# Optimization experiments

Measured on AMD Instinct MI355X. Metric: run time of the kernel, lower is better.

The kernel has to match this reference:

```python
import jax, jax.numpy as jnp
import numpy as np


def setup_inputs() -> dict:
    key = jax.random.key(0)
    k1, k2, k3, k4 = jax.random.split(key, 4)
    b, c_in, t, h, w = 8, 64, 16, 64, 64
    c_out, kh, kw = 64, 3, 3
    x = jax.random.normal(k1, (b, c_in, t, h, w), dtype=jnp.float32)
    alpha = jax.random.uniform(k2, (b, c_in, t, 1, 1), dtype=jnp.float32)
    fan_in = c_in * kh * kw
    weight = jax.random.normal(k3, (c_out, c_in, kh, kw), dtype=jnp.float32) / np.sqrt(fan_in)
    bias = jax.random.normal(k4, (c_out,), dtype=jnp.float32) * 0.05
    return {"x": x, "alpha": alpha, "weight": weight, "bias": bias}


def reference(x, alpha, weight, bias):
    # x: (b, c_in, t, h, w); alpha: (b, c_in, t, 1, 1)
    # weight: (c_out, c_in, kh, kw); bias: (c_out,)
    b, c_in, t, h, w = x.shape
    c_out, _, kh, kw = weight.shape
    pad = ((kh // 2, kh // 2), (kw // 2, kw // 2))  # padding=1 for 3x3
    # per-(b,t) calibrated weights: alpha scales the c_in dim (cal_dim='cin')
    a = jnp.transpose(alpha[..., 0, 0], (0, 2, 1))          # (b, t, c_in)
    w_bt = a[:, :, None, :, None, None] * weight[None, None]  # (b, t, c_out, c_in, kh, kw)
    xs = jnp.transpose(x, (0, 2, 1, 3, 4)).reshape(b * t, 1, c_in, h, w)
    ws = w_bt.reshape(b * t, c_out, c_in, kh, kw)

    def conv_one(xi, wi):
        return jax.lax.conv_general_dilated(
            xi, wi, window_strides=(1, 1), padding=pad,
            dimension_numbers=("NCHW", "OIHW", "NCHW"))[0]

    out = jax.vmap(conv_one)(xs, ws)                          # (b*t, c_out, h, w)
    out = out + bias[None, :, None, None]
    out = out.reshape(b, t, c_out, h, w).transpose(0, 2, 1, 3, 4)
    return out  # (b, c_out, t, h, w)
```

## Files before the change

### kernel.cpp

```cpp
#include <hip/hip_runtime.h>


#define CIN  64
#define COUT 64
#define TT   16
#define BB   8
#define HH   64
#define WW   64

typedef __attribute__((ext_vector_type(8))) short bf16x8;
typedef __attribute__((ext_vector_type(4))) float f32x4;

__device__ __forceinline__ unsigned short f2bf(float f) {
    union { float f; unsigned u; } v; v.f = f;
    unsigned r = (v.u + 0x7FFF + ((v.u >> 16) & 1)) >> 16;
    return (unsigned short)r;
}

__global__ __launch_bounds__(256) void prep_x(const float* __restrict__ x,
                                              const float* __restrict__ alpha,
                                              int4* __restrict__ xh) {
    __shared__ float ls[64 * 66];
    const int blk = blockIdx.x;
    const int h   = blk & 63;
    const int bt  = blk >> 6;
    const int t   = bt & 15;
    const int b   = bt >> 4;
    const int tid = threadIdx.x;

#pragma unroll
    for (int it = 0; it < 4; ++it) {
        int idx4 = tid + it * 256;
        int ci   = idx4 >> 4;
        int w4   = (idx4 & 15) * 4;
        float a  = alpha[(b * CIN + ci) * TT + t];
        const float* gp = x + (((b * CIN + ci) * TT + t) * HH + h) * WW + w4;
        float4 v = *(const float4*)gp;
        ls[(w4 + 0) * 66 + ci] = v.x * a;
        ls[(w4 + 1) * 66 + ci] = v.y * a;
        ls[(w4 + 2) * 66 + ci] = v.z * a;
        ls[(w4 + 3) * 66 + ci] = v.w * a;
    }
    __syncthreads();

#pragma unroll
    for (int it = 0; it < 2; ++it) {
        int tau  = tid + it * 256;
        int w    = tau >> 3;
        int slot = tau & 7;
        int g    = slot ^ (w & 7);
        const float* p = &ls[w * 66 + g * 8];
        float2 p0 = *(const float2*)(p + 0);
        float2 p1 = *(const float2*)(p + 2);
        float2 p2 = *(const float2*)(p + 4);
        float2 p3 = *(const float2*)(p + 6);
        int4 o;
        o.x = (int)f2bf(p0.x) | ((int)f2bf(p0.y) << 16);
        o.y = (int)f2bf(p1.x) | ((int)f2bf(p1.y) << 16);
        o.z = (int)f2bf(p2.x) | ((int)f2bf(p2.y) << 16);
        o.w = (int)f2bf(p3.x) | ((int)f2bf(p3.y) << 16);
        xh[((bt * 64 + h) * 64 + w) * 8 + slot] = o;
    }
}

__global__ __launch_bounds__(256) void prep_w(const float* __restrict__ wgt,
                                              unsigned short* __restrict__ wb) {
    int idx = blockIdx.x * 256 + threadIdx.x;
    if (idx < COUT * CIN * 9) {
        int co  = idx / (CIN * 9);
        int r   = idx - co * (CIN * 9);
        int ci  = r / 9;
        int tap = r - ci * 9;
        int slot = (ci >> 3) ^ (co & 7);
        wb[((tap * COUT + co) * 8 + slot) * 8 + (ci & 7)] = f2bf(wgt[idx]);
    }
}

__global__ __launch_bounds__(256) void conv2(const short* __restrict__ xh,
                                             const short* __restrict__ wb,
                                             const float* __restrict__ bias,
                                             float* __restrict__ out) {
    __shared__ __align__(16) short xs[4][66 * 64];
    __shared__ __align__(16) short wl[2][64 * 64];

    const int blk   = blockIdx.x;
    const int ytile = blk & 31;
    const int bt    = blk >> 5;
    const int t     = bt & 15;
    const int b     = bt >> 4;
    const int y0    = ytile * 2;
    const int tid   = threadIdx.x;
    const int wave  = tid >> 6;
    const int lane  = tid & 63;

    {
        const int r  = wave;
        const int gy = y0 - 1 + r;
        int4* dst = (int4*)xs[r];
        if ((unsigned)gy < HH) {
            const int4* src = (const int4*)(xh + (bt * 64 + gy) * 64 * 64);
            int4* d = (int4*)(xs[r] + 64);
#pragma unroll
            for (int it = 0; it < 8; ++it) d[it * 64 + lane] = src[it * 64 + lane];
            int4 z = {0, 0, 0, 0};
            if (lane < 8)       dst[lane] = z;
            else if (lane < 16) ((int4*)(xs[r] + 4160))[lane - 8] = z;
        } else {
            int4 z = {0, 0, 0, 0};
#pragma unroll
            for (int it = 0; it < 9; ++it) {
                int idx = it * 64 + lane;
                if (idx < 528) dst[idx] = z;
            }
        }
    }
    {
        const int4* src = (const int4*)wb;
        int4* d = (int4*)wl[0];
        d[tid] = src[tid];
        d[tid + 256] = src[tid + 256];
    }
    __syncthreads();

    f32x4 acc[4][2] = {};
    const int ywave = wave >> 1;
    const int wseg  = (wave & 1) * 32;
    const int co_l  = lane & 15;
    const int kg    = lane >> 4;

    for (int tap = 0; tap < 9; ++tap) {
        const int cur = tap & 1;
        int4 wp0, wp1;
        if (tap < 8) {
            const int4* src = (const int4*)(wb + (tap + 1) * 4096);
            wp0 = src[tid];
            wp1 = src[tid + 256];
        }
        const int ky = tap / 3;
        const int dx = (tap - 3 * ky) - 1;
        const short* xrow = xs[ywave + ky];
        const short* wcur = wl[cur];

#pragma unroll
        for (int kc = 0; kc < 2; ++kc) {
            const int g = kc * 4 + kg;
            bf16x8 af[4];
#pragma unroll
            for (int m = 0; m < 4; ++m) {
                int co   = m * 16 + co_l;
                int slot = g ^ (co & 7);
                af[m] = *(const bf16x8*)(wcur + co * 64 + slot * 8);
            }
            bf16x8 bfr[2];
#pragma unroll
            for (int nt = 0; nt < 2; ++nt) {
                int w    = wseg + nt * 16 + co_l;
                int wx   = w + dx;
                int slot = g ^ (wx & 7);
                bfr[nt] = *(const bf16x8*)(xrow + (wx + 1) * 64 + slot * 8);
            }
#pragma unroll
            for (int m = 0; m < 4; ++m)
#pragma unroll
                for (int nt = 0; nt < 2; ++nt)
                    acc[m][nt] = __builtin_amdgcn_mfma_f32_16x16x32_bf16(
                        af[m], bfr[nt], acc[m][nt], 0, 0, 0);
        }

        if (tap < 8) {
            int4* d = (int4*)wl[cur ^ 1];
            d[tid] = wp0;
            d[tid + 256] = wp1;
        }
        __syncthreads();
    }

    const int y = y0 + ywave;
#pragma unroll
    for (int m = 0; m < 4; ++m) {
#pragma unroll
        for (int r = 0; r < 4; ++r) {
            int co = m * 16 + (lane >> 4) * 4 + r;
            float bv = bias[co];
            float* op = out + (((b * COUT + co) * TT + t) * HH + y) * WW;
#pragma unroll
            for (int nt = 0; nt < 2; ++nt) {
                int w = wseg + nt * 16 + co_l;
                op[w] = acc[m][nt][r] + bv;
            }
        }
    }
}

extern "C" void kernel_launch(void* const* d_in, const int* in_sizes, int n_in,
                              void* d_out, int out_size, void* d_ws, size_t ws_size,
                              hipStream_t stream) {
    const float* x      = (const float*)d_in[0];
    const float* alpha  = (const float*)d_in[1];
    const float* weight = (const float*)d_in[2];
    const float* bias   = (const float*)d_in[3];
    float* out          = (float*)d_out;

    unsigned short* wb = (unsigned short*)d_ws;
    short* xhat = (short*)((char*)d_ws + (128 << 10));

    hipLaunchKernelGGL(prep_w, dim3(144), dim3(256), 0, stream, weight, wb);
    hipLaunchKernelGGL(prep_x, dim3(BB * TT * HH), dim3(256), 0, stream,
                       x, alpha, (int4*)xhat);
    hipLaunchKernelGGL(conv2, dim3(BB * TT * (HH / 2)), dim3(256), 0, stream,
                       xhat, (const short*)wb, bias, out);
}
```

Baseline: 284.5 us.

## Keep conv weights in registers and process four output rows per block

The conv kernel now loads each wave's full weight slice (all 9 taps, 32 output channels) into registers once, then loops over four output rows instead of two. This removes the shared-memory weight double-buffering and the per-tap barriers. Weights are stored unswizzled in global memory and read directly. prep_x changes its LDS row stride to 67 and uses scalar reads, to cut bank conflicts. The trade-off is heavy register pressure from 36 bf16x8 fragments under launch_bounds(256,2), a sequential per-row loop with fewer accumulators per wave, and half as many blocks.

```diff
diff --git a/kernel.cpp b/kernel.cpp
--- a/kernel.cpp
+++ b/kernel.cpp
@@ -11,16 +11,15 @@
 typedef __attribute__((ext_vector_type(8))) short bf16x8;
 typedef __attribute__((ext_vector_type(4))) float f32x4;
 
-__device__ __forceinline__ unsigned short f2bf(float f) {
+__device__ __forceinline__ unsigned int f2bf(float f) {
     union { float f; unsigned u; } v; v.f = f;
-    unsigned r = (v.u + 0x7FFF + ((v.u >> 16) & 1)) >> 16;
-    return (unsigned short)r;
+    return (v.u + 0x7FFF + ((v.u >> 16) & 1)) >> 16;
 }
 
 __global__ __launch_bounds__(256) void prep_x(const float* __restrict__ x,
                                               const float* __restrict__ alpha,
                                               int4* __restrict__ xh) {
-    __shared__ float ls[64 * 66];
+    __shared__ float ls[64 * 67];
     const int blk = blockIdx.x;
     const int h   = blk & 63;
     const int bt  = blk >> 6;
@@ -36,10 +35,10 @@
         float a  = alpha[(b * CIN + ci) * TT + t];
         const float* gp = x + (((b * CIN + ci) * TT + t) * HH + h) * WW + w4;
         float4 v = *(const float4*)gp;
-        ls[(w4 + 0) * 66 + ci] = v.x * a;
-        ls[(w4 + 1) * 66 + ci] = v.y * a;
-        ls[(w4 + 2) * 66 + ci] = v.z * a;
-        ls[(w4 + 3) * 66 + ci] = v.w * a;
+        ls[(w4 + 0) * 67 + ci] = v.x * a;
+        ls[(w4 + 1) * 67 + ci] = v.y * a;
+        ls[(w4 + 2) * 67 + ci] = v.z * a;
+        ls[(w4 + 3) * 67 + ci] = v.w * a;
     }
     __syncthreads();
 
@@ -49,16 +48,12 @@
         int w    = tau >> 3;
         int slot = tau & 7;
         int g    = slot ^ (w & 7);
-        const float* p = &ls[w * 66 + g * 8];
-        float2 p0 = *(const float2*)(p + 0);
-        float2 p1 = *(const float2*)(p + 2);
-        float2 p2 = *(const float2*)(p + 4);
-        float2 p3 = *(const float2*)(p + 6);
+        const float* p = &ls[w * 67 + g * 8];
         int4 o;
-        o.x = (int)f2bf(p0.x) | ((int)f2bf(p0.y) << 16);
-        o.y = (int)f2bf(p1.x) | ((int)f2bf(p1.y) << 16);
-        o.z = (int)f2bf(p2.x) | ((int)f2bf(p2.y) << 16);
-        o.w = (int)f2bf(p3.x) | ((int)f2bf(p3.y) << 16);
+        o.x = (int)(f2bf(p[0]) | (f2bf(p[1]) << 16));
+        o.y = (int)(f2bf(p[2]) | (f2bf(p[3]) << 16));
+        o.z = (int)(f2bf(p[4]) | (f2bf(p[5]) << 16));
+        o.w = (int)(f2bf(p[6]) | (f2bf(p[7]) << 16));
         xh[((bt * 64 + h) * 64 + w) * 8 + slot] = o;
     }
 }
@@ -71,122 +66,92 @@
         int r   = idx - co * (CIN * 9);
         int ci  = r / 9;
         int tap = r - ci * 9;
-        int slot = (ci >> 3) ^ (co & 7);
-        wb[((tap * COUT + co) * 8 + slot) * 8 + (ci & 7)] = f2bf(wgt[idx]);
+        wb[(tap * COUT + co) * CIN + ci] = (unsigned short)f2bf(wgt[idx]);
     }
 }
 
-__global__ __launch_bounds__(256) void conv2(const short* __restrict__ xh,
-                                             const short* __restrict__ wb,
-                                             const float* __restrict__ bias,
-                                             float* __restrict__ out) {
-    __shared__ __align__(16) short xs[4][66 * 64];
-    __shared__ __align__(16) short wl[2][64 * 64];
+__global__ __launch_bounds__(256, 2) void conv2(const short* __restrict__ xh,
+                                                const short* __restrict__ wb,
+                                                const float* __restrict__ bias,
+                                                float* __restrict__ out) {
+    __shared__ __align__(16) short xs[6 * 4224];
 
     const int blk   = blockIdx.x;
-    const int ytile = blk & 31;
-    const int bt    = blk >> 5;
+    const int ytile = blk & 15;
+    const int bt    = blk >> 4;
     const int t     = bt & 15;
     const int b     = bt >> 4;
-    const int y0    = ytile * 2;
+    const int y0    = ytile * 4;
     const int tid   = threadIdx.x;
     const int wave  = tid >> 6;
     const int lane  = tid & 63;
+    const int lane15 = lane & 15;
+    const int laneh  = lane >> 4;
+    const int mh    = wave >> 1;
+    const int nh    = wave & 1;
 
-    {
-        const int r  = wave;
-        const int gy = y0 - 1 + r;
-        int4* dst = (int4*)xs[r];
-        if ((unsigned)gy < HH) {
-            const int4* src = (const int4*)(xh + (bt * 64 + gy) * 64 * 64);
-            int4* d = (int4*)(xs[r] + 64);
+    for (int tsk = tid; tsk < 6 * 528; tsk += 256) {
+        int r  = tsk / 528;
+        int i  = tsk - r * 528;
+        int gy = y0 - 1 + r;
+        int4 v = {0, 0, 0, 0};
+        if ((unsigned)gy < (unsigned)HH) {
+            int j = i - 8;
+            if ((unsigned)j < 512u)
+                v = ((const int4*)xh)[(bt * 64 + gy) * 512 + j];
+        }
+        ((int4*)xs)[r * 528 + i] = v;
+    }
+
+    bf16x8 af[36];
 #pragma unroll
-            for (int it = 0; it < 8; ++it) d[it * 64 + lane] = src[it * 64 + lane];
-            int4 z = {0, 0, 0, 0};
-            if (lane < 8)       dst[lane] = z;
-            else if (lane < 16) ((int4*)(xs[r] + 4160))[lane - 8] = z;
-        } else {
-            int4 z = {0, 0, 0, 0};
+    for (int s = 0; s < 18; ++s) {
+        const int tap = s >> 1;
+        const int kc  = s & 1;
+        const int ci0 = kc * 32 + laneh * 8;
 #pragma unroll
-            for (int it = 0; it < 9; ++it) {
-                int idx = it * 64 + lane;
-                if (idx < 528) dst[idx] = z;
-            }
+        for (int mi = 0; mi < 2; ++mi) {
+            int co = mh * 32 + mi * 16 + lane15;
+            af[s * 2 + mi] = *(const bf16x8*)(wb + (tap * COUT + co) * CIN + ci0);
         }
-    }
-    {
-        const int4* src = (const int4*)wb;
-        int4* d = (int4*)wl[0];
-        d[tid] = src[tid];
-        d[tid + 256] = src[tid + 256];
     }
     __syncthreads();
 
-    f32x4 acc[4][2] = {};
-    const int ywave = wave >> 1;
-    const int wseg  = (wave & 1) * 32;
-    const int co_l  = lane & 15;
-    const int kg    = lane >> 4;
-
-    for (int tap = 0; tap < 9; ++tap) {
-        const int cur = tap & 1;
-        int4 wp0, wp1;
-        if (tap < 8) {
-            const int4* src = (const int4*)(wb + (tap + 1) * 4096);
-            wp0 = src[tid];
-            wp1 = src[tid + 256];
-        }
-        const int ky = tap / 3;
-        const int dx = (tap - 3 * ky) - 1;
-        const short* xrow = xs[ywave + ky];
-        const short* wcur = wl[cur];
-
+    for (int y = 0; y < 4; ++y) {
+        f32x4 acc[2][2] = {};
 #pragma unroll
-        for (int kc = 0; kc < 2; ++kc) {
-            const int g = kc * 4 + kg;
-            bf16x8 af[4];
-#pragma unroll
-            for (int m = 0; m < 4; ++m) {
-                int co   = m * 16 + co_l;
-                int slot = g ^ (co & 7);
-                af[m] = *(const bf16x8*)(wcur + co * 64 + slot * 8);
-            }
+        for (int s = 0; s < 18; ++s) {
+            const int tap = s >> 1;
+            const int kc  = s & 1;
+            const int ky  = tap / 3;
+            const int dx  = (tap - 3 * ky) - 1;
+            const short* xrow = xs + (y + ky) * 4224;
             bf16x8 bfr[2];
 #pragma unroll
             for (int nt = 0; nt < 2; ++nt) {
-                int w    = wseg + nt * 16 + co_l;
+                int w    = nh * 32 + nt * 16 + lane15;
                 int wx   = w + dx;
-                int slot = g ^ (wx & 7);
+                int slot = (kc * 4 + laneh) ^ (wx & 7);
                 bfr[nt] = *(const bf16x8*)(xrow + (wx + 1) * 64 + slot * 8);
             }
 #pragma unroll
-            for (int m = 0; m < 4; ++m)
+            for (int mi = 0; mi < 2; ++mi)
 #pragma unroll
                 for (int nt = 0; nt < 2; ++nt)
-                    acc[m][nt] = __builtin_amdgcn_mfma_f32_16x16x32_bf16(
-                        af[m], bfr[nt], acc[m][nt], 0, 0, 0);
+                    acc[mi][nt] = __builtin_amdgcn_mfma_f32_16x16x32_bf16(
+                        af[s * 2 + mi], bfr[nt], acc[mi][nt], 0, 0, 0);
         }
-
-        if (tap < 8) {
-            int4* d = (int4*)wl[cur ^ 1];
-            d[tid] = wp0;
-            d[tid + 256] = wp1;
-        }
-        __syncthreads();
-    }
-
-    const int y = y0 + ywave;
+        const int gy = y0 + y;
 #pragma unroll
-    for (int m = 0; m < 4; ++m) {
+        for (int mi = 0; mi < 2; ++mi) {
 #pragma unroll
-        for (int r = 0; r < 4; ++r) {
-            int co = m * 16 + (lane >> 4) * 4 + r;
-            float bv = bias[co];
-            float* op = out + (((b * COUT + co) * TT + t) * HH + y) * WW;
+            for (int r = 0; r < 4; ++r) {
+                int co = mh * 32 + mi * 16 + laneh * 4 + r;
+                float bv = bias[co];
+                float* op = out + (((b * COUT + co) * TT + t) * HH + gy) * WW;
 #pragma unroll
-            for (int nt = 0; nt < 2; ++nt) {
-                int w = wseg + nt * 16 + co_l;
-                op[w] = acc[m][nt][r] + bv;
+                for (int nt = 0; nt < 2; ++nt)
+                    op[nh * 32 + nt * 16 + lane15] = acc[mi][nt][r] + bv;
             }
         }
     }
@@ -207,6 +172,6 @@
     hipLaunchKernelGGL(prep_w, dim3(144), dim3(256), 0, stream, weight, wb);
     hipLaunchKernelGGL(prep_x, dim3(BB * TT * HH), dim3(256), 0, stream,
                        x, alpha, (int4*)xhat);
-    hipLaunchKernelGGL(conv2, dim3(BB * TT * (HH / 2)), dim3(256), 0, stream,
+    hipLaunchKernelGGL(conv2, dim3(BB * TT * (HH / 4)), dim3(256), 0, stream,
                        xhat, (const short*)wb, bias, out);
 }
```

Measured after the change: 303.7 us. 6.7% more time.
